# Optimization experiments

Hardware: AMD Instinct MI355X
Metric: run time of the kernel (lower is better)

The kernel has to match this reference:

```python
import jax, jax.numpy as jnp
from jax import lax
import numpy as np

D_MODEL = 1024
D_STATE = 16
D_CONV = 4
EXPAND = 2
D_INNER = EXPAND * D_MODEL
DT_RANK = -(-D_MODEL // D_STATE)  # ceil(d_model/d_state) = 64
BATCH, SEQ = 2, 2048


def setup_inputs() -> dict:
    key = jax.random.key(0)
    ks = jax.random.split(key, 12)
    s = lambda fan_in: 1.0 / np.sqrt(fan_in)
    inp = {
        "x": jax.random.normal(ks[0], (BATCH, SEQ, D_MODEL), jnp.float32),
        # weights stored as [in, out] (i.e. torch W.T) for y = x @ W + b
        "in_proj_w": jax.random.normal(ks[1], (D_MODEL, 2 * D_INNER), jnp.float32) * s(D_MODEL),
        "in_proj_b": jax.random.normal(ks[2], (2 * D_INNER,), jnp.float32) * s(D_MODEL),
        # depthwise conv weight in torch Conv1d layout [out_ch, in_ch/groups=1, k]
        "conv_w": jax.random.normal(ks[3], (D_INNER, 1, D_CONV), jnp.float32) * s(D_CONV),
        "conv_b": jax.random.normal(ks[4], (D_INNER,), jnp.float32) * s(D_CONV),
        "x_proj_w": jax.random.normal(ks[5], (D_INNER, DT_RANK + 2 * D_STATE), jnp.float32) * s(D_INNER),
        "dt_proj_w": jax.random.normal(ks[6], (DT_RANK, D_INNER), jnp.float32) * s(DT_RANK),
        "dt_proj_b": jax.random.normal(ks[7], (D_INNER,), jnp.float32) * s(DT_RANK),
        # log_A = log(arange(1, d_state+1)) repeated over d_inner rows
        "log_A": jnp.log(jnp.broadcast_to(jnp.arange(1, D_STATE + 1, dtype=jnp.float32), (D_INNER, D_STATE))),
        "D": jnp.ones((D_INNER,), jnp.float32),
        "out_proj_w": jax.random.normal(ks[8], (D_INNER, D_MODEL), jnp.float32) * s(D_INNER),
        "out_proj_b": jax.random.normal(ks[9], (D_MODEL,), jnp.float32) * s(D_INNER),
    }
    return inp


def reference(x, in_proj_w, in_proj_b, conv_w, conv_b, x_proj_w,
              dt_proj_w, dt_proj_b, log_A, D, out_proj_w, out_proj_b):
    batch, seq_len, _ = x.shape
    d_inner, d_state = log_A.shape
    d_conv = conv_w.shape[-1]
    dt_rank = dt_proj_w.shape[0]

    xr = x @ in_proj_w + in_proj_b                      # [B, L, 2*d_inner]
    x_val, res = jnp.split(xr, 2, axis=-1)

    # depthwise causal conv: torch pads both sides by d_conv-1 then keeps first L
    # outputs, which equals left-padding by d_conv-1.
    xv = x_val.transpose(0, 2, 1)                       # [B, C, L]
    xv = lax.conv_general_dilated(xv, conv_w, window_strides=(1,),
                                  padding=[(d_conv - 1, 0)],
                                  feature_group_count=d_inner)
    xv = xv + conv_b[None, :, None]
    x_val = jax.nn.silu(xv.transpose(0, 2, 1))          # [B, L, d_inner]

    x_dbl = x_val @ x_proj_w                            # [B, L, dt_rank + 2*d_state]
    dt = x_dbl[..., :dt_rank]
    Bm = x_dbl[..., dt_rank:dt_rank + d_state]          # [B, L, N]
    Cm = x_dbl[..., dt_rank + d_state:]                 # [B, L, N]
    dt = jax.nn.softplus(dt @ dt_proj_w + dt_proj_b)    # [B, L, d_inner]

    A = -jnp.exp(log_A)                                 # [d_inner, N]

    def step(h, inputs):
        dt_t, B_t, C_t, x_t = inputs                    # [B,d], [B,N], [B,N], [B,d]
        dA = jnp.exp(dt_t[:, :, None] * A)              # [B, d_inner, N]
        h = dA * h + (dt_t * x_t)[:, :, None] * B_t[:, None, :]
        y_t = jnp.einsum('bdn,bn->bd', h, C_t)
        return h, y_t

    h0 = jnp.zeros((batch, d_inner, d_state), x.dtype)
    xs = (dt.transpose(1, 0, 2), Bm.transpose(1, 0, 2),
          Cm.transpose(1, 0, 2), x_val.transpose(1, 0, 2))
    _, ys = lax.scan(step, h0, xs)                      # ys: [L, B, d_inner]

    y = ys.transpose(1, 0, 2) + x_val * D
    return (y * jax.nn.silu(res)) @ out_proj_w + out_proj_b
```

## Files before the change

kernel.cpp:

```cpp
#include <hip/hip_runtime.h>
#include <hip/hip_bf16.h>

#define BATCH 2
#define SEQ 2048
#define DM 1024
#define DI 2048
#define DS 16
#define DR 64
#define XPC 96
#define ROWS 4096
#define NC 32
#define CL 64
#define XRLD 4096
#define KSXP 8

typedef __attribute__((ext_vector_type(8))) short bf16x8;
typedef __attribute__((ext_vector_type(4))) float f32x4;
typedef unsigned short ushort_t;
typedef unsigned int u32;

#define GLD_LDS16(g, l) \
    __builtin_amdgcn_global_load_lds((const __attribute__((address_space(1))) u32*)(g), \
                                     (__attribute__((address_space(3))) u32*)(l), 16, 0, 0)

static __device__ __forceinline__ float bf2f(ushort_t u) {
    __hip_bfloat16 b = *(__hip_bfloat16*)&u;
    return __bfloat162float(b);
}
static __device__ __forceinline__ ushort_t f2bf(float f) {
    __hip_bfloat16 b = __float2bfloat16(f);
    return *(ushort_t*)&b;
}

__global__ __launch_bounds__(256) void cvt_f32_bf16(
    const float* __restrict__ in, ushort_t* __restrict__ out)
{
    const size_t i = (size_t)(blockIdx.x * 256 + threadIdx.x) * 4;
    float4 v = *(const float4*)(in + i);
    ushort4 o;
    o.x = f2bf(v.x); o.y = f2bf(v.y); o.z = f2bf(v.z); o.w = f2bf(v.w);
    *(ushort4*)(out + i) = o;
}

__global__ __launch_bounds__(256) void convt_multi(
    const float* __restrict__ ipw, ushort_t* __restrict__ wt_in,
    const float* __restrict__ opw, ushort_t* __restrict__ wt_out,
    const float* __restrict__ xpw, ushort_t* __restrict__ wt_xp,
    const float* __restrict__ dpw, ushort_t* __restrict__ wt_dt)
{
    __shared__ float t[32][33];
    int b = blockIdx.x;
    const float* W; ushort_t* Wt; int K, N, nb;
    if (b < 4096)      { W = ipw; Wt = wt_in;  K = 1024; N = 4096; nb = 128; }
    else if (b < 6144) { b -= 4096; W = opw; Wt = wt_out; K = 2048; N = 1024; nb = 32; }
    else if (b < 6336) { b -= 6144; W = xpw; Wt = wt_xp;  K = 2048; N = 96;   nb = 3;  }
    else               { b -= 6336; W = dpw; Wt = wt_dt;  K = 64;   N = 2048; nb = 64; }
    const int n0 = (b % nb) * 32, k0 = (b / nb) * 32;
    const int tx = threadIdx.x & 31, ty = threadIdx.x >> 5;
#pragma unroll
    for (int i = 0; i < 32; i += 8)
        t[ty + i][tx] = W[(size_t)(k0 + ty + i) * N + n0 + tx];
    __syncthreads();
#pragma unroll
    for (int i = 0; i < 32; i += 8)
        Wt[(size_t)(n0 + ty + i) * K + k0 + tx] = f2bf(t[tx][ty + i]);
}

template<int EPI, typename OutT, int SPLITK>
__global__ __launch_bounds__(256) void gemm128_bt(
    const ushort_t* __restrict__ A, const ushort_t* __restrict__ Bt,
    const float* __restrict__ bias, OutT* __restrict__ C,
    int K, int ldc)
{
    __shared__ ushort_t As[2][128 * 32];
    __shared__ ushort_t Bs[2][128 * 32];
    const int tid = threadIdx.x;
    const int lane = tid & 63, wid = tid >> 6;
    const int quad = lane >> 4, l16 = lane & 15;
    const int wr = wid >> 1, wc = wid & 1;
    const int nbx = gridDim.x / SPLITK;
    const int bn = blockIdx.x % nbx;
    const int ks = blockIdx.x / nbx;
    const int bm = blockIdx.y;
    const int ksl = K / SPLITK;
    const int kbeg = ks * ksl;
    OutT* Cb = C + (size_t)ks * (size_t)gridDim.y * 128 * ldc;

    const int sr = tid >> 2, sk = (tid & 3) << 3;
    const ushort_t* Ag0 = A + (size_t)(bm * 128 + sr) * K + kbeg + sk;
    const ushort_t* Ag1 = A + (size_t)(bm * 128 + 64 + sr) * K + kbeg + sk;
    const ushort_t* Bg0 = Bt + (size_t)(bn * 128 + sr) * K + kbeg + sk;
    const ushort_t* Bg1 = Bt + (size_t)(bn * 128 + 64 + sr) * K + kbeg + sk;

    f32x4 acc[4][4];
#pragma unroll
    for (int m = 0; m < 4; ++m)
#pragma unroll
        for (int n = 0; n < 4; ++n) acc[m][n] = (f32x4){0.f, 0.f, 0.f, 0.f};

    auto stage = [&](int buf, int kk) {
        GLD_LDS16(Ag0 + kk, &As[buf][tid * 8]);
        GLD_LDS16(Ag1 + kk, &As[buf][(tid + 256) * 8]);
        GLD_LDS16(Bg0 + kk, &Bs[buf][tid * 8]);
        GLD_LDS16(Bg1 + kk, &Bs[buf][(tid + 256) * 8]);
    };
    auto compute = [&](int buf) {
        bf16x8 a[4], b[4];
#pragma unroll
        for (int m = 0; m < 4; ++m)
            a[m] = *(const bf16x8*)&As[buf][(wr * 64 + m * 16 + l16) * 32 + 8 * quad];
#pragma unroll
        for (int n = 0; n < 4; ++n)
            b[n] = *(const bf16x8*)&Bs[buf][(wc * 64 + n * 16 + l16) * 32 + 8 * quad];
#pragma unroll
        for (int m = 0; m < 4; ++m)
#pragma unroll
            for (int n = 0; n < 4; ++n)
                acc[m][n] = __builtin_amdgcn_mfma_f32_16x16x32_bf16(
                    a[m], b[n], acc[m][n], 0, 0, 0);
    };

    const int nt = ksl >> 5;
    stage(0, 0);
    for (int t = 0; t < nt; t += 2) {
        __syncthreads();
        if (t + 1 < nt) stage(1, (t + 1) << 5);
        compute(0);
        __syncthreads();
        if (t + 2 < nt) stage(0, (t + 2) << 5);
        compute(1);
    }

#pragma unroll
    for (int m = 0; m < 4; ++m) {
        const int row0 = bm * 128 + wr * 64 + m * 16 + quad * 4;
#pragma unroll
        for (int n = 0; n < 4; ++n) {
            const int col = bn * 128 + wc * 64 + n * 16 + l16;
            const float bv = bias ? bias[col] : 0.f;
#pragma unroll
            for (int r = 0; r < 4; ++r) {
                float v = acc[m][n][r] + bv;
                if constexpr (EPI == 1) {
                    ((ushort_t*)Cb)[(size_t)(row0 + r) * ldc + col] = f2bf(v);
                } else if constexpr (EPI == 2) {
                    float sp = (v > 20.f) ? v : log1pf(__expf(v));
                    ((float*)Cb)[(size_t)(row0 + r) * ldc + col] = sp;
                } else if constexpr (EPI == 3) {
                    float sp = (v > 20.f) ? v : log1pf(__expf(v));
                    ((ushort_t*)Cb)[(size_t)(row0 + r) * ldc + col] = f2bf(sp);
                } else {
                    ((float*)Cb)[(size_t)(row0 + r) * ldc + col] = v;
                }
            }
        }
    }
}

__global__ __launch_bounds__(256) void sum2_bias(
    const float* __restrict__ part, const float* __restrict__ bias,
    float* __restrict__ out)
{
    const size_t i = (size_t)(blockIdx.x * 256 + threadIdx.x) * 4;
    float4 a = *(const float4*)(part + i);
    float4 b = *(const float4*)(part + (size_t)ROWS * DM + i);
    float4 bv = *(const float4*)(bias + (i & (DM - 1)));
    float4 o;
    o.x = a.x + b.x + bv.x; o.y = a.y + b.y + bv.y;
    o.z = a.z + b.z + bv.z; o.w = a.w + b.w + bv.w;
    *(float4*)(out + i) = o;
}

__global__ __launch_bounds__(256) void xproj_splitk(
    const ushort_t* __restrict__ A, const ushort_t* __restrict__ Bt,
    float* __restrict__ part, int K)
{
    const int BM = 64, BN = XPC;
    __shared__ ushort_t As[64 * 40];
    __shared__ ushort_t Bs[XPC * 40];
    const int tid = threadIdx.x;
    const int wid = tid >> 6, lane = tid & 63;
    const int quad = lane >> 4, l16 = lane & 15;
    const int wr = wid;
    const int bm = blockIdx.y;
    const int ks = blockIdx.x;
    const int kslc = K / KSXP;
    const int kbeg = ks * kslc;

    f32x4 acc[6];
#pragma unroll
    for (int n = 0; n < 6; ++n) acc[n] = (f32x4){0.f, 0.f, 0.f, 0.f};

    for (int k0 = kbeg; k0 < kbeg + kslc; k0 += 32) {
        for (int i = tid; i < BM * 4; i += 256) {
            int r = i >> 2, kk = (i & 3) << 3;
            *(uint4*)&As[r * 40 + kk] =
                *(const uint4*)&A[(size_t)(bm * BM + r) * K + k0 + kk];
        }
        for (int i = tid; i < BN * 4; i += 256) {
            int r = i >> 2, kk = (i & 3) << 3;
            *(uint4*)&Bs[r * 40 + kk] =
                *(const uint4*)&Bt[(size_t)r * K + k0 + kk];
        }
        __syncthreads();
        bf16x8 a, b[6];
        a = *(const bf16x8*)&As[(wr * 16 + l16) * 40 + 8 * quad];
#pragma unroll
        for (int n = 0; n < 6; ++n)
            b[n] = *(const bf16x8*)&Bs[(n * 16 + l16) * 40 + 8 * quad];
#pragma unroll
        for (int n = 0; n < 6; ++n)
            acc[n] = __builtin_amdgcn_mfma_f32_16x16x32_bf16(a, b[n], acc[n], 0, 0, 0);
        __syncthreads();
    }

    float* out = part + (size_t)ks * ROWS * XPC;
    const int row0 = bm * BM + wr * 16 + quad * 4;
#pragma unroll
    for (int n = 0; n < 6; ++n) {
        const int col = n * 16 + l16;
#pragma unroll
        for (int r = 0; r < 4; ++r)
            out[(size_t)(row0 + r) * XPC + col] = acc[n][r];
    }
}

__global__ __launch_bounds__(256) void xproj_reduce(
    const float* __restrict__ part, float* __restrict__ xdbl,
    ushort_t* __restrict__ xdt)
{
    const size_t i = (size_t)(blockIdx.x * 256 + threadIdx.x) * 4;
    float4 s = *(const float4*)(part + i);
#pragma unroll
    for (int ks = 1; ks < KSXP; ++ks) {
        float4 v = *(const float4*)(part + (size_t)ks * ROWS * XPC + i);
        s.x += v.x; s.y += v.y; s.z += v.z; s.w += v.w;
    }
    *(float4*)(xdbl + i) = s;
    const int col = (int)(i % XPC);
    if (col < DR) {
        const int row = (int)(i / XPC);
        ushort4 o;
        o.x = f2bf(s.x); o.y = f2bf(s.y); o.z = f2bf(s.z); o.w = f2bf(s.w);
        *(ushort4*)(xdt + (size_t)row * DR + col) = o;
    }
}

__global__ __launch_bounds__(256) void conv_silu_kernel(
    const ushort_t* __restrict__ xr, const float* __restrict__ cw,
    const float* __restrict__ cb, ushort_t* __restrict__ xc)
{
    const int i = blockIdx.x * 256 + threadIdx.x;
    const int r = i >> 9;
    const int d0 = (i & 511) << 2;
    const int t = r & (SEQ - 1);
    float w[4][4];
#pragma unroll
    for (int j = 0; j < 4; ++j)
        *(float4*)w[j] = *(const float4*)&cw[(d0 + j) * 4];
    float4 bb = *(const float4*)&cb[d0];
    float acc[4] = {bb.x, bb.y, bb.z, bb.w};
#pragma unroll
    for (int k = 0; k < 4; ++k) {
        int tt = t - 3 + k;
        if (tt >= 0) {
            ushort4 v = *(const ushort4*)&xr[(size_t)(r - 3 + k) * XRLD + d0];
            acc[0] += bf2f(v.x) * w[0][k];
            acc[1] += bf2f(v.y) * w[1][k];
            acc[2] += bf2f(v.z) * w[2][k];
            acc[3] += bf2f(v.w) * w[3][k];
        }
    }
    ushort4 o;
    o.x = f2bf(acc[0] / (1.f + __expf(-acc[0])));
    o.y = f2bf(acc[1] / (1.f + __expf(-acc[1])));
    o.z = f2bf(acc[2] / (1.f + __expf(-acc[2])));
    o.w = f2bf(acc[3] / (1.f + __expf(-acc[3])));
    *(ushort4*)&xc[(size_t)r * DI + d0] = o;
}


__global__ __launch_bounds__(256) void scan_pass1(
    const ushort_t* __restrict__ dt, const ushort_t* __restrict__ xc,
    const float* __restrict__ xdbl, const float* __restrict__ logA,
    float* __restrict__ hend, float* __restrict__ prodA)
{
    __shared__ float Bsm[CL][DS];
    const int bid = blockIdx.x;
    const int bc = bid >> 3;
    const int d = ((bid & 7) << 8) + threadIdx.x;
    const int c = bc & (NC - 1);
    const int b = bc >> 5;
    const int r0 = b * SEQ + c * CL;

    {
        int i = threadIdx.x;
        int r = i >> 2, n4 = (i & 3) << 2;
        *(float4*)&Bsm[r][n4] = *(const float4*)&xdbl[(size_t)(r0 + r) * XPC + DR + n4];
    }
    __syncthreads();

    float A[DS], h[DS];
#pragma unroll
    for (int n = 0; n < DS; ++n) {
        A[n] = -__expf(logA[d * DS + n]);
        h[n] = 0.f;
    }
    float dtsum = 0.f;
#pragma unroll 4
    for (int t = 0; t < CL; ++t) {
        const int r = r0 + t;
        float dtv = bf2f(dt[(size_t)r * DI + d]);
        float xv = bf2f(xc[(size_t)r * DI + d]);
        float bx = dtv * xv;
        dtsum += dtv;
#pragma unroll
        for (int n = 0; n < DS; ++n) {
            float dA = __expf(dtv * A[n]);
            h[n] = dA * h[n] + bx * Bsm[t][n];
        }
    }
#pragma unroll
    for (int n = 0; n < DS; ++n) {
        size_t o = ((size_t)bc * DS + n) * DI + d;
        hend[o] = h[n];
        prodA[o] = __expf(dtsum * A[n]);
    }
}

__global__ __launch_bounds__(256) void scan_pass2(
    const float* __restrict__ hend, const float* __restrict__ prodA,
    float* __restrict__ hin)
{
    const int gid = blockIdx.x * 256 + threadIdx.x;
    const int d = gid & (DI - 1);
    const int bn = gid >> 11;
    const int n = bn & (DS - 1);
    const int b = bn >> 4;
    float hprev = 0.f;
#pragma unroll 8
    for (int c = 0; c < NC; ++c) {
        size_t o = ((size_t)(b * NC + c) * DS + n) * DI + d;
        hin[o] = hprev;
        hprev = prodA[o] * hprev + hend[o];
    }
}

__global__ __launch_bounds__(256) void scan_pass3(
    const ushort_t* __restrict__ dt, const ushort_t* __restrict__ xc,
    const float* __restrict__ xdbl, const ushort_t* __restrict__ res,
    const float* __restrict__ logA, const float* __restrict__ Dp,
    const float* __restrict__ hin, ushort_t* __restrict__ yg)
{
    __shared__ float BCs[CL][2 * DS];
    const int bid = blockIdx.x;
    const int bc = bid >> 3;
    const int d = ((bid & 7) << 8) + threadIdx.x;
    const int c = bc & (NC - 1);
    const int b = bc >> 5;
    const int r0 = b * SEQ + c * CL;

    {
        int i = threadIdx.x;
        int r = i >> 3, c4 = (i & 7) << 2;
        *(float4*)&BCs[r][c4] = *(const float4*)&xdbl[(size_t)(r0 + r) * XPC + DR + c4];
        int i2 = i + 256;
        int r2 = i2 >> 3, c42 = (i2 & 7) << 2;
        *(float4*)&BCs[r2][c42] = *(const float4*)&xdbl[(size_t)(r0 + r2) * XPC + DR + c42];
    }
    __syncthreads();

    float A[DS], h[DS];
#pragma unroll
    for (int n = 0; n < DS; ++n) {
        A[n] = -__expf(logA[d * DS + n]);
        h[n] = hin[((size_t)bc * DS + n) * DI + d];
    }
    const float Dd = Dp[d];
#pragma unroll 4
    for (int t = 0; t < CL; ++t) {
        const int r = r0 + t;
        float dtv = bf2f(dt[(size_t)r * DI + d]);
        float xv = bf2f(xc[(size_t)r * DI + d]);
        float bx = dtv * xv;
        float y = 0.f;
#pragma unroll
        for (int n = 0; n < DS; ++n) {
            float dA = __expf(dtv * A[n]);
            h[n] = dA * h[n] + bx * BCs[t][n];
            y += h[n] * BCs[t][DS + n];
        }
        y += xv * Dd;
        float rv = bf2f(res[(size_t)r * XRLD + d]);
        float sr = rv / (1.f + __expf(-rv));
        yg[(size_t)r * DI + d] = f2bf(y * sr);
    }
}

extern "C" void kernel_launch(void* const* d_in, const int* in_sizes, int n_in,
                              void* d_out, int out_size, void* d_ws, size_t ws_size,
                              hipStream_t stream) {
    const float* x          = (const float*)d_in[0];
    const float* in_proj_w  = (const float*)d_in[1];
    const float* in_proj_b  = (const float*)d_in[2];
    const float* conv_w     = (const float*)d_in[3];
    const float* conv_b     = (const float*)d_in[4];
    const float* x_proj_w   = (const float*)d_in[5];
    const float* dt_proj_w  = (const float*)d_in[6];
    const float* dt_proj_b  = (const float*)d_in[7];
    const float* log_A      = (const float*)d_in[8];
    const float* Dp         = (const float*)d_in[9];
    const float* out_proj_w = (const float*)d_in[10];
    const float* out_proj_b = (const float*)d_in[11];

    float* ws    = (float*)d_ws;
    float*    part  = ws;
    ushort_t* dt_bf = (ushort_t*)ws;
    float* xdbl  = ws    + (size_t)ROWS * DI;
    float* hend  = xdbl  + (size_t)ROWS * XPC;
    float* prodA = hend  + (size_t)BATCH * NC * DS * DI;
    float* hin   = prodA + (size_t)BATCH * NC * DS * DI;
    float* part_out = hend;
    ushort_t* xr     = (ushort_t*)(hin + (size_t)BATCH * NC * DS * DI);
    ushort_t* xc_bf  = xr     + (size_t)ROWS * XRLD;
    ushort_t* yg_bf  = xc_bf  + (size_t)ROWS * DI;
    ushort_t* x_bf   = yg_bf  + (size_t)ROWS * DI;
    ushort_t* wt_in  = x_bf   + (size_t)ROWS * DM;
    ushort_t* wt_out = wt_in  + (size_t)2 * DI * DM;
    ushort_t* wt_xp  = wt_out + (size_t)DM * DI;
    ushort_t* wt_dt  = wt_xp  + (size_t)XPC * DI;
    ushort_t* xdt_bf = wt_dt  + (size_t)DI * DR;

    dim3 blk(256);

    cvt_f32_bf16<<<(ROWS * DM / 4) / 256, blk, 0, stream>>>(x, x_bf);
    convt_multi<<<6464, blk, 0, stream>>>(in_proj_w, wt_in, out_proj_w, wt_out,
                                          x_proj_w, wt_xp, dt_proj_w, wt_dt);

    gemm128_bt<1, ushort_t, 1><<<dim3(XRLD / 128, ROWS / 128), blk, 0, stream>>>(
        x_bf, wt_in, in_proj_b, xr, DM, XRLD);

    conv_silu_kernel<<<(ROWS * DI / 4) / 256, blk, 0, stream>>>(xr, conv_w, conv_b, xc_bf);

    xproj_splitk<<<dim3(KSXP, ROWS / 64), blk, 0, stream>>>(xc_bf, wt_xp, part, DI);
    xproj_reduce<<<(ROWS * XPC / 4) / 256, blk, 0, stream>>>(part, xdbl, xdt_bf);

    gemm128_bt<3, ushort_t, 1><<<dim3(DI / 128, ROWS / 128), blk, 0, stream>>>(
        xdt_bf, wt_dt, dt_proj_b, dt_bf, DR, DI);

    scan_pass1<<<BATCH * NC * (DI / 256), blk, 0, stream>>>(
        dt_bf, xc_bf, xdbl, log_A, hend, prodA);
    scan_pass2<<<(BATCH * DS * DI) / 256, blk, 0, stream>>>(hend, prodA, hin);
    scan_pass3<<<BATCH * NC * (DI / 256), blk, 0, stream>>>(
        dt_bf, xc_bf, xdbl, xr + DI, log_A, Dp, hin, yg_bf);

    gemm128_bt<0, float, 2><<<dim3(2 * DM / 128, ROWS / 128), blk, 0, stream>>>(
        yg_bf, wt_out, nullptr, part_out, DI, DM);
    sum2_bias<<<(ROWS * DM / 4) / 256, blk, 0, stream>>>(
        part_out, out_proj_b, (float*)d_out);
}
```

Baseline: 277.5 us.

## Triple-buffer GEMM LDS staging with vmcnt waits and conflict-free fragment layout

Switches the bf16 MFMA GEMM from double to triple LDS buffering. Loads run two k-tiles ahead, gated by explicit s_waitcnt vmcnt counters and a single barrier per iteration instead of two. The global-to-LDS mapping also changes so each wave's 16x8 fragment is stored contiguously, which is meant to cut LDS bank conflicts on the bf16x8 reads. In exchange LDS use grows by half, which may reduce occupancy, and correctness relies on the hand-written vmcnt counts.

```diff
diff --git a/kernel.cpp b/kernel.cpp
--- a/kernel.cpp
+++ b/kernel.cpp
@@ -72,8 +72,8 @@
     const float* __restrict__ bias, OutT* __restrict__ C,
     int K, int ldc)
 {
-    __shared__ ushort_t As[2][128 * 32];
-    __shared__ ushort_t Bs[2][128 * 32];
+    __shared__ ushort_t As[3][128 * 32];
+    __shared__ ushort_t Bs[3][128 * 32];
     const int tid = threadIdx.x;
     const int lane = tid & 63, wid = tid >> 6;
     const int quad = lane >> 4, l16 = lane & 15;
@@ -86,11 +86,12 @@
     const int kbeg = ks * ksl;
     OutT* Cb = C + (size_t)ks * (size_t)gridDim.y * 128 * ldc;
 
-    const int sr = tid >> 2, sk = (tid & 3) << 3;
-    const ushort_t* Ag0 = A + (size_t)(bm * 128 + sr) * K + kbeg + sk;
-    const ushort_t* Ag1 = A + (size_t)(bm * 128 + 64 + sr) * K + kbeg + sk;
-    const ushort_t* Bg0 = Bt + (size_t)(bn * 128 + sr) * K + kbeg + sk;
-    const ushort_t* Bg1 = Bt + (size_t)(bn * 128 + 64 + sr) * K + kbeg + sk;
+    const int sf = tid >> 6, sq = (tid >> 4) & 3, sl = tid & 15;
+    const int koff = sq * 8;
+    const ushort_t* Ag0 = A + (size_t)(bm * 128 + sf * 16 + sl) * K + kbeg + koff;
+    const ushort_t* Ag1 = Ag0 + (size_t)64 * K;
+    const ushort_t* Bg0 = Bt + (size_t)(bn * 128 + sf * 16 + sl) * K + kbeg + koff;
+    const ushort_t* Bg1 = Bg0 + (size_t)64 * K;
 
     f32x4 acc[4][4];
 #pragma unroll
@@ -98,20 +99,20 @@
 #pragma unroll
         for (int n = 0; n < 4; ++n) acc[m][n] = (f32x4){0.f, 0.f, 0.f, 0.f};
 
-    auto stage = [&](int buf, int kk) {
-        GLD_LDS16(Ag0 + kk, &As[buf][tid * 8]);
-        GLD_LDS16(Ag1 + kk, &As[buf][(tid + 256) * 8]);
-        GLD_LDS16(Bg0 + kk, &Bs[buf][tid * 8]);
-        GLD_LDS16(Bg1 + kk, &Bs[buf][(tid + 256) * 8]);
+    auto stage = [&](int buf, int kelem) {
+        GLD_LDS16(Ag0 + kelem, &As[buf][tid * 8]);
+        GLD_LDS16(Ag1 + kelem, &As[buf][(tid + 256) * 8]);
+        GLD_LDS16(Bg0 + kelem, &Bs[buf][tid * 8]);
+        GLD_LDS16(Bg1 + kelem, &Bs[buf][(tid + 256) * 8]);
     };
     auto compute = [&](int buf) {
         bf16x8 a[4], b[4];
 #pragma unroll
         for (int m = 0; m < 4; ++m)
-            a[m] = *(const bf16x8*)&As[buf][(wr * 64 + m * 16 + l16) * 32 + 8 * quad];
+            a[m] = *(const bf16x8*)&As[buf][((wr * 4 + m) * 4 + quad) * 128 + l16 * 8];
 #pragma unroll
         for (int n = 0; n < 4; ++n)
-            b[n] = *(const bf16x8*)&Bs[buf][(wc * 64 + n * 16 + l16) * 32 + 8 * quad];
+            b[n] = *(const bf16x8*)&Bs[buf][((wc * 4 + n) * 4 + quad) * 128 + l16 * 8];
 #pragma unroll
         for (int m = 0; m < 4; ++m)
 #pragma unroll
@@ -122,13 +123,15 @@
 
     const int nt = ksl >> 5;
     stage(0, 0);
-    for (int t = 0; t < nt; t += 2) {
-        __syncthreads();
-        if (t + 1 < nt) stage(1, (t + 1) << 5);
-        compute(0);
-        __syncthreads();
-        if (t + 2 < nt) stage(0, (t + 2) << 5);
-        compute(1);
+    stage(1, 32);
+    for (int t = 0; t < nt; ++t) {
+        const int buf = t % 3;
+        if (t + 1 < nt) asm volatile("s_waitcnt vmcnt(4)" ::: "memory");
+        else            asm volatile("s_waitcnt vmcnt(0)" ::: "memory");
+        __builtin_amdgcn_s_barrier();
+        __builtin_amdgcn_sched_barrier(0);
+        if (t + 2 < nt) stage((t + 2) % 3, (t + 2) << 5);
+        compute(buf);
     }
 
 #pragma unroll
```

Result: slower. 316.2 us (+14.0%).
